# Performance work log

Measured on AMD Instinct MI355X. Metric: run time of the kernel, lower is better.

The kernel has to match this reference:

```python
import jax, jax.numpy as jnp
import numpy as np

B, S, D = 128, 512, 240
E, TOP_K = 8, 2


def setup_inputs() -> dict:
    key = jax.random.key(0)
    k1, k2, k3 = jax.random.split(key, 3)
    x = jax.random.normal(k1, (B, S, D), dtype=jnp.float32)
    gate_w = jax.random.normal(k2, (D, E), dtype=jnp.float32) * 0.02
    gate_b = jnp.zeros((E,), dtype=jnp.float32)
    # torch Linear weight is [out, in]; store as [E, D_out, D_in]
    expert_w = jax.random.normal(k3, (E, D, D), dtype=jnp.float32) * 0.02
    expert_b = jnp.zeros((E, D), dtype=jnp.float32)
    return {"x": x, "gate_w": gate_w, "gate_b": gate_b,
            "expert_w": expert_w, "expert_b": expert_b}


def reference(x, gate_w, gate_b, expert_w, expert_b):
    # Gating
    gate_logits = jnp.einsum('bsd,de->bse', x, gate_w) + gate_b      # [B,S,E]
    gate_weights = jax.nn.softmax(gate_logits, axis=-1)
    top_w, top_idx = jax.lax.top_k(gate_weights, TOP_K)              # [B,S,K]
    top_w = top_w / jnp.sum(top_w, axis=-1, keepdims=True)
    # Combine weights per expert: [B,S,E]
    combine = jnp.sum(jax.nn.one_hot(top_idx, E, dtype=x.dtype) * top_w[..., None], axis=-2)
    # Dense all-expert compute (same math as masked dispatch):
    # expert_out[b,s,e,f] = x[b,s,:] @ expert_w[e].T + expert_b[e]
    expert_out = jnp.einsum('bsd,efd->bsef', x, expert_w) + expert_b  # [B,S,E,D]
    out = jnp.einsum('bsef,bse->bsf', expert_out, combine)            # [B,S,D]
    return out
```

## Files before the change

kernel.cpp:

```cpp
#include <hip/hip_runtime.h>
#include <cstdint>

#define NTOK 65536
#define DIM 240
#define KP 256
#define NMETA 576
#define NGB 1024

typedef short bf16x8 __attribute__((ext_vector_type(8)));
typedef float f32x16 __attribute__((ext_vector_type(16)));

union U16B { uint4 u; bf16x8 v; };

__device__ __forceinline__ unsigned short f2bf(float x) {
  unsigned int u = __float_as_uint(x);
  u += 0x7fffu + ((u >> 16) & 1u);
  return (unsigned short)(u >> 16);
}

template<int CTRL>
__device__ __forceinline__ float dppf(float v) {
  return __int_as_float(__builtin_amdgcn_update_dpp(0, __float_as_int(v), CTRL, 0xF, 0xF, true));
}
template<int CTRL>
__device__ __forceinline__ unsigned dppu(unsigned v) {
  return (unsigned)__builtin_amdgcn_update_dpp(0, (int)v, CTRL, 0xF, 0xF, true);
}
__device__ __forceinline__ bool pgt(unsigned a, unsigned b) {
  float fa = __uint_as_float(a & ~7u), fb = __uint_as_float(b & ~7u);
  return (fa != fb) ? (fa > fb) : ((a & 7u) < (b & 7u));
}
template<int CTRL>
__device__ __forceinline__ void top2round(unsigned& a1, unsigned& a2) {
  unsigned b1 = dppu<CTRL>(a1), b2 = dppu<CTRL>(a2);
  bool g = pgt(a1, b1);
  unsigned n1 = g ? a1 : b1;
  unsigned lo = g ? b1 : a1;
  unsigned m2 = pgt(a2, b2) ? a2 : b2;
  a2 = pgt(lo, m2) ? lo : m2;
  a1 = n1;
}

__global__ __launch_bounds__(256) void prep_w(const float* __restrict__ ew,
                                              unsigned short* __restrict__ WbT) {
  int idx = blockIdx.x * 256 + threadIdx.x;
  int k0 = (idx & 63) << 2;
  int n  = (idx >> 6) & 255;
  int e  = idx >> 14;
  ushort4 v = {0, 0, 0, 0};
  if (n < DIM && k0 < DIM) {
    const float* wrow = ew + (e * DIM + n) * DIM;
    v.x = f2bf(wrow[k0]); v.y = f2bf(wrow[k0 + 1]);
    v.z = f2bf(wrow[k0 + 2]); v.w = f2bf(wrow[k0 + 3]);
  }
  *(ushort4*)&WbT[((size_t)(e * 32 + (k0 >> 3)) * 256 + n) * 8 + (k0 & 7)] = v;
}

__global__ __launch_bounds__(512) void gating(const float* __restrict__ x,
                                              const float* __restrict__ gw,
                                              const float* __restrict__ gb,
                                              unsigned short* __restrict__ xb,
                                              unsigned char* __restrict__ pairid,
                                              float2* __restrict__ wpair,
                                              int* __restrict__ hist2d) {
  __shared__ __align__(16) float gwT[8][DIM];
  __shared__ int hist[64];
  for (int i = threadIdx.x; i < 8 * DIM; i += 512) gwT[i & 7][i >> 3] = gw[i];
  if (threadIdx.x < 64) hist[threadIdx.x] = 0;
  __syncthreads();
  const int lane = threadIdx.x & 63;
  const int w = threadIdx.x >> 6;
  const bool act = lane < 60;
  float4 g[8];
#pragma unroll
  for (int e = 0; e < 8; ++e)
    g[e] = act ? *(const float4*)(&gwT[e][lane * 4]) : make_float4(0.f, 0.f, 0.f, 0.f);
  const int elane = 4 * (lane & 1) + 2 * ((lane >> 1) & 1) + ((lane >> 3) & 1);
  const float gbl = gb[elane];
  const int tbase = blockIdx.x * 64 + w * 8;
  for (int it = 0; it < 8; ++it) {
    const int t = tbase + it;
    float4 xv = act ? *(const float4*)(x + (size_t)t * DIM + lane * 4)
                    : make_float4(0.f, 0.f, 0.f, 0.f);
    float p[8];
#pragma unroll
    for (int e = 0; e < 8; ++e)
      p[e] = xv.x * g[e].x + xv.y * g[e].y + xv.z * g[e].z + xv.w * g[e].w;
    float q4[4];
#pragma unroll
    for (int i = 0; i < 4; ++i) {
      float lo = p[i] + dppf<0xB1>(p[i]);
      float hi = p[i + 4] + dppf<0xB1>(p[i + 4]);
      q4[i] = (lane & 1) ? hi : lo;
    }
    float q2[2];
#pragma unroll
    for (int i = 0; i < 2; ++i) {
      float lo = q4[i] + dppf<0x4E>(q4[i]);
      float hi = q4[i + 2] + dppf<0x4E>(q4[i + 2]);
      q2[i] = (lane & 2) ? hi : lo;
    }
    float lo = q2[0] + dppf<0x128>(q2[0]);
    float hi = q2[1] + dppf<0x128>(q2[1]);
    float s = (lane & 8) ? hi : lo;
    s += __shfl_xor(s, 4);
    s += __shfl_xor(s, 16);
    s += __shfl_xor(s, 32);
    s += gbl;
    unsigned a1 = (__float_as_uint(s) & ~7u) | (unsigned)elane;
    unsigned a2 = (0xFF800000u & ~7u) | 7u;
    top2round<0xB1>(a1, a2);
    top2round<0x4E>(a1, a2);
    top2round<0x128>(a1, a2);
    ushort4 v = {0, 0, 0, 0};
    if (act) { v.x = f2bf(xv.x); v.y = f2bf(xv.y); v.z = f2bf(xv.z); v.w = f2bf(xv.w); }
    *(ushort4*)(xb + (size_t)t * KP + lane * 4) = v;
    if (lane == 0) {
      const int i1 = a1 & 7, i2 = a2 & 7;
      const float l1 = __uint_as_float(a1 & ~7u), l2 = __uint_as_float(a2 & ~7u);
      const float qq = expf(l2 - l1);
      const float w1 = 1.f / (1.f + qq);
      const float w2 = qq / (1.f + qq);
      const int ea = (i1 < i2) ? i1 : i2, eb2 = (i1 < i2) ? i2 : i1;
      const float wa = (i1 < i2) ? w1 : w2, wb2 = (i1 < i2) ? w2 : w1;
      const int pp = ea * 8 + eb2;
      pairid[t] = (unsigned char)pp;
      wpair[t] = make_float2(wa, wb2);
      atomicAdd(&hist[pp], 1);
    }
  }
  __syncthreads();
  if (threadIdx.x < 64) hist2d[blockIdx.x * 64 + threadIdx.x] = hist[threadIdx.x];
}

__global__ __launch_bounds__(1024) void scan1_k(const int* __restrict__ hist2d,
                                                int* __restrict__ lbase2d,
                                                int* __restrict__ cnt) {
  __shared__ int s[NGB];
  const int p = blockIdx.x, tid = threadIdx.x;
  const int v = hist2d[tid * 64 + p];
  s[tid] = v;
  __syncthreads();
  for (int off = 1; off < NGB; off <<= 1) {
    int tv = (tid >= off) ? s[tid - off] : 0;
    __syncthreads();
    s[tid] += tv;
    __syncthreads();
  }
  lbase2d[tid * 64 + p] = s[tid] - v;
  if (tid == NGB - 1) cnt[p] = s[tid];
}

__global__ void scan2_k(const int* __restrict__ cnt, int* __restrict__ start,
                        int4* __restrict__ meta) {
  __shared__ int sc[64], sstart[64], stile[64], stot;
  const int tid = threadIdx.x;
  sc[tid] = cnt[tid];
  __syncthreads();
  if (tid == 0) {
    int a = 0, ta = 0;
    for (int p = 0; p < 64; ++p) { sstart[p] = a; stile[p] = ta; a += sc[p]; ta += (sc[p] + 127) >> 7; }
    stot = ta;
  }
  __syncthreads();
  start[tid] = sstart[tid];
  const int c = sc[tid], e0 = tid >> 3, e1 = tid & 7;
  for (int i = 0; (i << 7) < c; ++i)
    meta[stile[tid] + i] = make_int4(e0, e1, sstart[tid] + (i << 7), min(128, c - (i << 7)));
  for (int j = stot + tid; j < NMETA; j += 64)
    meta[j] = make_int4(0, 0, 0, 0);
}

__global__ __launch_bounds__(64) void route_k(const unsigned char* __restrict__ pairid,
                                              const float2* __restrict__ wpair,
                                              const int* __restrict__ start,
                                              const int* __restrict__ lbase2d,
                                              float2* __restrict__ wsorted,
                                              int* __restrict__ tokord) {
  __shared__ int lcnt[64];
  const int b = blockIdx.x, tid = threadIdx.x;
  lcnt[tid] = 0;
  __syncthreads();
  const int t = b * 64 + tid;
  const int p = pairid[t];
  const int rank = atomicAdd(&lcnt[p], 1);
  const int pos = start[p] + lbase2d[b * 64 + p] + rank;
  wsorted[pos] = wpair[t];
  tokord[pos] = t;
}

#define GLDS16(g, l)                                                        \
  __builtin_amdgcn_global_load_lds(                                         \
      (__attribute__((address_space(1))) unsigned int*)(g),                 \
      (__attribute__((address_space(3))) unsigned int*)(l), 16, 0, 0)

__global__ __launch_bounds__(512, 2) void moe_gemm_pair(const unsigned short* __restrict__ xb,
                                                        const unsigned short* __restrict__ WbT,
                                                        const float* __restrict__ ebias,
                                                        const float2* __restrict__ wsorted,
                                                        const int* __restrict__ tokord,
                                                        const int4* __restrict__ meta,
                                                        float* __restrict__ out) {
  extern __shared__ __align__(16) char smem[];
  int* ptok = (int*)(smem + 122880);
  float2* wab = (float2*)(smem + 123392);

  const int4 m = meta[blockIdx.x];
  const int n = m.w;
  if (n == 0) return;
  const int tid = threadIdx.x, lane = tid & 63, wid = tid >> 6;
  const int tq = wid >> 1, chf = wid & 1;
  const int l31 = lane & 31, hi = lane >> 5;

  if (tid < 128) {
    const int idx = m.z + (tid < n ? tid : n - 1);
    ptok[tid] = tokord[idx];
    wab[tid] = wsorted[idx];
  }
  __syncthreads();

  const char* ab = (const char*)xb + (size_t)ptok[tq * 32 + l31] * 512 + hi * 16;
  uint4 a[15];
#pragma unroll
  for (int it = 0; it < 15; ++it) a[it] = *(const uint4*)(ab + it * 32);

  const char* wsA = (const char*)WbT + (size_t)m.x * 131072 + tid * 16;
#pragma unroll
  for (int j = 0; j < 15; ++j) GLDS16(wsA + j * 8192, smem + tid * 16 + j * 8192);
  __syncthreads();

  f32x16 accA[4] = {}, accB[4] = {};
  const char* wrd = smem + ((chf * 128 + l31) << 4);

#pragma unroll
  for (int it = 0; it < 15; ++it) {
    U16B av; av.u = a[it];
    const char* wg = wrd + ((2 * it + hi) << 12);
#pragma unroll
    for (int cf = 0; cf < 4; ++cf) {
      U16B b; b.u = *(const uint4*)(wg + cf * 512);
      accA[cf] = __builtin_amdgcn_mfma_f32_32x32x16_bf16(av.v, b.v, accA[cf], 0, 0, 0);
    }
  }
  __syncthreads();

  const char* wsB = (const char*)WbT + (size_t)m.y * 131072 + tid * 16;
#pragma unroll
  for (int j = 0; j < 15; ++j) GLDS16(wsB + j * 8192, smem + tid * 16 + j * 8192);
  __syncthreads();

#pragma unroll
  for (int it = 0; it < 15; ++it) {
    U16B av; av.u = a[it];
    const char* wg = wrd + ((2 * it + hi) << 12);
#pragma unroll
    for (int cf = 0; cf < 4; ++cf) {
      U16B b; b.u = *(const uint4*)(wg + cf * 512);
      accB[cf] = __builtin_amdgcn_mfma_f32_32x32x16_bf16(av.v, b.v, accB[cf], 0, 0, 0);
    }
  }

#pragma unroll
  for (int cf = 0; cf < 4; ++cf) {
    const int col = chf * 128 + cf * 32 + l31;
    if (col < DIM) {
      const float be0 = ebias[m.x * DIM + col];
      const float be1 = ebias[m.y * DIM + col];
#pragma unroll
      for (int r = 0; r < 16; ++r) {
        const int rw = tq * 32 + (r & 3) + ((r >> 2) << 3) + (hi << 2);
        if (rw < n) {
          const float2 w2 = wab[rw];
          out[(size_t)ptok[rw] * DIM + col] =
              w2.x * (accA[cf][r] + be0) + w2.y * (accB[cf][r] + be1);
        }
      }
    }
  }
}

extern "C" void kernel_launch(void* const* d_in, const int* in_sizes, int n_in,
                              void* d_out, int out_size, void* d_ws, size_t ws_size,
                              hipStream_t stream) {
  const float* x  = (const float*)d_in[0];
  const float* gw = (const float*)d_in[1];
  const float* gb = (const float*)d_in[2];
  const float* ew = (const float*)d_in[3];
  const float* eb = (const float*)d_in[4];
  float* out = (float*)d_out;

  char* ws = (char*)d_ws;
  unsigned short* WbT  = (unsigned short*)ws;
  unsigned short* xb   = (unsigned short*)(ws + 1048576);
  float2*         wpr  = (float2*)(ws + 34734080);
  float2*         wsr  = (float2*)(ws + 35258368);
  int*            tord = (int*)(ws + 35784704);
  unsigned char*  pid  = (unsigned char*)(ws + 36047872);
  int*            h2d  = (int*)(ws + 36113408);
  int*            lb2d = (int*)(ws + 36375552);
  int*            cnt  = (int*)(ws + 36637696);
  int*            strt = (int*)(ws + 36637952);
  int4*           meta = (int4*)(ws + 36638208);

  hipFuncSetAttribute((const void*)moe_gemm_pair, hipFuncAttributeMaxDynamicSharedMemorySize, 124416);

  prep_w<<<512, 256, 0, stream>>>(ew, WbT);
  gating<<<NGB, 512, 0, stream>>>(x, gw, gb, xb, pid, wpr, h2d);
  scan1_k<<<64, NGB, 0, stream>>>(h2d, lb2d, cnt);
  scan2_k<<<1, 64, 0, stream>>>(cnt, strt, meta);
  route_k<<<NGB, 64, 0, stream>>>(pid, wpr, strt, lb2d, wsr, tord);
  moe_gemm_pair<<<NMETA, 512, 124416, stream>>>(xb, WbT, eb, wsr, tord, meta, out);
}
```

Before: 106.9 us.

## Split MoE pair GEMM by output column halves, stage tokens in LDS, stream weights

The grouped GEMM now launches two blocks per pair tile, each computing half of the output columns. Token activations are staged into LDS with global_load_lds. Both experts' weight fragments are read from global memory straight into registers with double buffering, so the two separate weight-staging phases and their barriers go away. LDS use shrinks from about 124KB to about 67KB and the launch bound allows four blocks per CU, which should raise occupancy and overlap. The cost is that each token tile's activations are loaded twice, once per column half, and weights are read from global/L2 without LDS reuse.

```diff
diff --git a/kernel.cpp b/kernel.cpp
--- a/kernel.cpp
+++ b/kernel.cpp
@@ -194,7 +194,7 @@
       (__attribute__((address_space(1))) unsigned int*)(g),                 \
       (__attribute__((address_space(3))) unsigned int*)(l), 16, 0, 0)
 
-__global__ __launch_bounds__(512, 2) void moe_gemm_pair(const unsigned short* __restrict__ xb,
+__global__ __launch_bounds__(512, 4) void moe_gemm_pair(const unsigned short* __restrict__ xb,
                                                         const unsigned short* __restrict__ WbT,
                                                         const float* __restrict__ ebias,
                                                         const float2* __restrict__ wsorted,
@@ -202,14 +202,15 @@
                                                         const int4* __restrict__ meta,
                                                         float* __restrict__ out) {
   extern __shared__ __align__(16) char smem[];
-  int* ptok = (int*)(smem + 122880);
-  float2* wab = (float2*)(smem + 123392);
-
-  const int4 m = meta[blockIdx.x];
+  int* ptok = (int*)(smem + 65536);
+  float2* wab = (float2*)(smem + 66048);
+
+  const int4 m = meta[blockIdx.x >> 1];
   const int n = m.w;
   if (n == 0) return;
+  const int ch = blockIdx.x & 1;
   const int tid = threadIdx.x, lane = tid & 63, wid = tid >> 6;
-  const int tq = wid >> 1, chf = wid & 1;
+  const int tq = wid >> 1, cg = wid & 1;
   const int l31 = lane & 31, hi = lane >> 5;
 
   if (tid < 128) {
@@ -219,50 +220,49 @@
   }
   __syncthreads();
 
-  const char* ab = (const char*)xb + (size_t)ptok[tq * 32 + l31] * 512 + hi * 16;
-  uint4 a[15];
-#pragma unroll
-  for (int it = 0; it < 15; ++it) a[it] = *(const uint4*)(ab + it * 32);
-
-  const char* wsA = (const char*)WbT + (size_t)m.x * 131072 + tid * 16;
-#pragma unroll
-  for (int j = 0; j < 15; ++j) GLDS16(wsA + j * 8192, smem + tid * 16 + j * 8192);
-  __syncthreads();
-
-  f32x16 accA[4] = {}, accB[4] = {};
-  const char* wrd = smem + ((chf * 128 + l31) << 4);
-
-#pragma unroll
-  for (int it = 0; it < 15; ++it) {
-    U16B av; av.u = a[it];
-    const char* wg = wrd + ((2 * it + hi) << 12);
-#pragma unroll
-    for (int cf = 0; cf < 4; ++cf) {
-      U16B b; b.u = *(const uint4*)(wg + cf * 512);
-      accA[cf] = __builtin_amdgcn_mfma_f32_32x32x16_bf16(av.v, b.v, accA[cf], 0, 0, 0);
-    }
-  }
-  __syncthreads();
-
-  const char* wsB = (const char*)WbT + (size_t)m.y * 131072 + tid * 16;
-#pragma unroll
-  for (int j = 0; j < 15; ++j) GLDS16(wsB + j * 8192, smem + tid * 16 + j * 8192);
-  __syncthreads();
-
-#pragma unroll
-  for (int it = 0; it < 15; ++it) {
-    U16B av; av.u = a[it];
-    const char* wg = wrd + ((2 * it + hi) << 12);
-#pragma unroll
-    for (int cf = 0; cf < 4; ++cf) {
-      U16B b; b.u = *(const uint4*)(wg + cf * 512);
-      accB[cf] = __builtin_amdgcn_mfma_f32_32x32x16_bf16(av.v, b.v, accB[cf], 0, 0, 0);
-    }
-  }
-
-#pragma unroll
-  for (int cf = 0; cf < 4; ++cf) {
-    const int col = chf * 128 + cf * 32 + l31;
+  const int colb = ch * 128 + cg * 64 + l31;
+  const char* wbase0 = (const char*)WbT + (size_t)m.x * 131072 + (size_t)hi * 4096 + (size_t)colb * 16;
+  const char* wbase1 = (const char*)WbT + (size_t)m.y * 131072 + (size_t)hi * 4096 + (size_t)colb * 16;
+
+  uint4 w0[4], w1[4];
+  w0[0] = *(const uint4*)(wbase0);
+  w0[1] = *(const uint4*)(wbase1);
+  w0[2] = *(const uint4*)(wbase0 + 512);
+  w0[3] = *(const uint4*)(wbase1 + 512);
+
+#pragma unroll
+  for (int j = 0; j < 8; ++j) {
+    const int i = tid + 512 * j;
+    GLDS16((const char*)xb + (size_t)ptok[i & 127] * 512 + (i >> 7) * 16, smem + i * 16);
+  }
+  __syncthreads();
+
+  f32x16 accA[2] = {}, accB[2] = {};
+  const char* apt = smem + (size_t)hi * 2048 + (size_t)(tq * 32 + l31) * 16;
+
+#pragma unroll
+  for (int it = 0; it < 16; ++it) {
+    if (it < 15) {
+      const size_t o = (size_t)(it + 1) * 8192;
+      uint4* nxt = (it & 1) ? w0 : w1;
+      nxt[0] = *(const uint4*)(wbase0 + o);
+      nxt[1] = *(const uint4*)(wbase1 + o);
+      nxt[2] = *(const uint4*)(wbase0 + o + 512);
+      nxt[3] = *(const uint4*)(wbase1 + o + 512);
+    }
+    const uint4* cur = (it & 1) ? w1 : w0;
+    U16B a; a.u = *(const uint4*)(apt + (size_t)it * 4096);
+    U16B b0, b1, b2, b3;
+    b0.u = cur[0]; b1.u = cur[1]; b2.u = cur[2]; b3.u = cur[3];
+    accA[0] = __builtin_amdgcn_mfma_f32_32x32x16_bf16(a.v, b0.v, accA[0], 0, 0, 0);
+    accB[0] = __builtin_amdgcn_mfma_f32_32x32x16_bf16(a.v, b1.v, accB[0], 0, 0, 0);
+    accA[1] = __builtin_amdgcn_mfma_f32_32x32x16_bf16(a.v, b2.v, accA[1], 0, 0, 0);
+    accB[1] = __builtin_amdgcn_mfma_f32_32x32x16_bf16(a.v, b3.v, accB[1], 0, 0, 0);
+  }
+
+#pragma unroll
+  for (int cf = 0; cf < 2; ++cf) {
+    const int col = ch * 128 + cg * 64 + cf * 32 + l31;
     if (col < DIM) {
       const float be0 = ebias[m.x * DIM + col];
       const float be1 = ebias[m.y * DIM + col];
@@ -302,12 +302,12 @@
   int*            strt = (int*)(ws + 36637952);
   int4*           meta = (int4*)(ws + 36638208);
 
-  hipFuncSetAttribute((const void*)moe_gemm_pair, hipFuncAttributeMaxDynamicSharedMemorySize, 124416);
+  hipFuncSetAttribute((const void*)moe_gemm_pair, hipFuncAttributeMaxDynamicSharedMemorySize, 67072);
 
   prep_w<<<512, 256, 0, stream>>>(ew, WbT);
   gating<<<NGB, 512, 0, stream>>>(x, gw, gb, xb, pid, wpr, h2d);
   scan1_k<<<64, NGB, 0, stream>>>(h2d, lb2d, cnt);
   scan2_k<<<1, 64, 0, stream>>>(cnt, strt, meta);
   route_k<<<NGB, 64, 0, stream>>>(pid, wpr, strt, lb2d, wsr, tord);
-  moe_gemm_pair<<<NMETA, 512, 124416, stream>>>(xb, WbT, eb, wsr, tord, meta, out);
-}
+  moe_gemm_pair<<<2 * NMETA, 512, 67072, stream>>>(xb, WbT, eb, wsr, tord, meta, out);
+}
```

New measurement: 103.0 us. 3.7% less time.
